# Performance work log

Hardware: AMD Instinct MI355X
Metric: run time of the kernel (lower is better)

The kernel has to match this reference:

```python
import jax, jax.numpy as jnp
import numpy as np

D = 128       # embedding dim; n_phi == D is forced by the module (n_phi = phi.shape[0])
NE = 8192     # enroll trials
NT = 8192     # test trials
EPS = 1e-8


def _make_params():
    """Replicates GPLDA.__init__: derive Q_hat, lambda, U_k from phi/sigma via pinv+SVD."""
    rng = np.random.default_rng(0)
    phi = rng.normal(size=(D, D)) * 0.1
    A = rng.normal(size=(D, D))
    sigma = np.eye(D) + 0.01 * (A @ A.T)          # SPD noise covariance
    sigma_ac = phi @ phi.T
    sigma_tot = sigma_ac + sigma
    inv_tot = np.linalg.pinv(sigma_tot)
    inv_sigma = np.linalg.pinv(sigma_tot - sigma_ac @ inv_tot @ sigma_ac)
    Q = inv_tot - inv_sigma
    P = inv_tot @ sigma_ac @ inv_sigma
    U, S, _ = np.linalg.svd(P)
    n_phi = D
    U_k = U[:, :n_phi]                            # (D, n_phi)
    Q_hat = U_k.T @ Q @ U_k                       # (n_phi, n_phi)
    lam = S[:n_phi]                               # diag of lambda_v
    W = rng.normal(size=(D, D)) / np.sqrt(D)      # whitening matrix
    miu = rng.normal(size=(D,))                   # global mean
    return W, miu, lam, U_k, Q_hat


def setup_inputs() -> dict:
    key = jax.random.key(0)
    k1, k2 = jax.random.split(key)
    W, miu, lam, U_k, Q_hat = _make_params()
    f32 = jnp.float32
    return {
        "x_enroll": jax.random.normal(k1, (NE, D), dtype=f32),
        "x_test": jax.random.normal(k2, (NT, D), dtype=f32),
        "W": jnp.asarray(W, f32),
        "miu": jnp.asarray(miu, f32),
        "lam": jnp.asarray(lam, f32),
        "U_k": jnp.asarray(U_k, f32),
        "Q_hat": jnp.asarray(Q_hat, f32),
    }


def _project(x, miu, W, U_k):
    # x: (N, D) -> projected (n_phi, N)
    xt = x.T - miu[:, None]                       # (D, N) per-feature mean subtraction
    norm = jnp.sqrt(jnp.sum(xt * xt, axis=0))     # per-sample L2 norm (over features)
    xt = xt / (norm + EPS)                        # length-normalize each column
    return U_k.T @ (W.T @ xt)                     # (n_phi, N)


def reference(x_enroll, x_test, W, miu, lam, U_k, Q_hat):
    xe = _project(x_enroll, miu, W, U_k)          # (n_phi, NE)
    xt = _project(x_test, miu, W, U_k)            # (n_phi, NT)
    # diag(xe.T @ Q_hat @ xe) without forming the NxN product
    score_h1 = jnp.sum(xe * (Q_hat @ xe), axis=0)               # (NE,)
    score_h2 = jnp.sum(xt * (Q_hat @ xt), axis=0)               # (NT,)
    # 2 * xe.T @ diag(lam) @ xt
    score_h1h2 = 2.0 * jnp.einsum('kn,k,km->nm', xe, lam, xt)   # (NE, NT)
    return score_h1h2 + score_h1[:, None] + score_h2[None, :]
```

## Files before the change

kernel.cpp:

```cpp
#include <hip/hip_runtime.h>
#include <math.h>

#define D 128
#define NE 8192
#define NT 8192
#define KEXT 384
#define SB 16

typedef __bf16 bf16x8 __attribute__((ext_vector_type(8)));
typedef float f32x4 __attribute__((ext_vector_type(4)));

__device__ __forceinline__ unsigned short f32_to_bf16(float f) {
  unsigned int u = __float_as_uint(f);
  u += 0x7FFFu + ((u >> 16) & 1u);
  return (unsigned short)(u >> 16);
}
__device__ __forceinline__ float bf16_to_f32(unsigned short h) {
  return __uint_as_float(((unsigned int)h) << 16);
}

#define GLOAD_LDS16(g, l)                                                      \
  __builtin_amdgcn_global_load_lds(                                            \
      (__attribute__((address_space(1))) const void*)(g),                      \
      (__attribute__((address_space(3))) void*)(l), 16, 0, 0)

__global__ __launch_bounds__(128) void prep_M(const float* __restrict__ W,
                                              const float* __restrict__ U,
                                              float* __restrict__ M) {
  const int d = blockIdx.x;
  const int k = threadIdx.x;
  const float* Wr = W + d * D;
  float acc = 0.f;
#pragma unroll 8
  for (int c = 0; c < D; ++c) acc += Wr[c] * U[c * D + k];
  M[d * D + k] = acc;
}

__global__ __launch_bounds__(128) void project_kernel(
    const float* __restrict__ Xe, const float* __restrict__ Xt,
    const float* __restrict__ miu, const float* __restrict__ M,
    const float* __restrict__ Qh, const float* __restrict__ lam,
    unsigned short* __restrict__ Aext, unsigned short* __restrict__ Bext,
    float* __restrict__ s1, float* __restrict__ s2) {
  const int t = threadIdx.x;
  const int mode = blockIdx.y;
  const int n0 = blockIdx.x * SB;
  const float* X = mode ? Xt : Xe;
  unsigned short* Ext = mode ? Bext : Aext;
  float* sc = mode ? s2 : s1;

  __shared__ __align__(16) float V[D][20];
  __shared__ __align__(16) float Y[D][20];
  __shared__ float rn[SB];

  const float mu = miu[t];
#pragma unroll
  for (int i = 0; i < SB; ++i)
    V[t][i] = X[(size_t)(n0 + i) * D + t] - mu;
  __syncthreads();

  if (t < SB) {
    float s = 0.f;
#pragma unroll 8
    for (int d = 0; d < D; ++d) { float v = V[d][t]; s += v * v; }
    rn[t] = 1.0f / (sqrtf(s) + 1e-8f);
  }
  __syncthreads();

  float y[SB];
#pragma unroll
  for (int s = 0; s < SB; ++s) y[s] = 0.f;
  {
    const float* Mc = M + t;
#pragma unroll 4
    for (int d = 0; d < D; ++d) {
      float m = Mc[d * D];
#pragma unroll
      for (int s4 = 0; s4 < SB / 4; ++s4) {
        float4 v = *(const float4*)&V[d][s4 * 4];
        y[s4 * 4 + 0] += m * v.x;
        y[s4 * 4 + 1] += m * v.y;
        y[s4 * 4 + 2] += m * v.z;
        y[s4 * 4 + 3] += m * v.w;
      }
    }
  }
#pragma unroll
  for (int s = 0; s < SB; ++s) y[s] *= rn[s];

#pragma unroll
  for (int s4 = 0; s4 < SB / 4; ++s4) {
    float4 v;
    v.x = y[s4 * 4 + 0]; v.y = y[s4 * 4 + 1];
    v.z = y[s4 * 4 + 2]; v.w = y[s4 * 4 + 3];
    *(float4*)&Y[t][s4 * 4] = v;
  }
  __syncthreads();

  float z[SB];
#pragma unroll
  for (int s = 0; s < SB; ++s) z[s] = 0.f;
  {
    const float* Qc = Qh + t;
#pragma unroll 4
    for (int d = 0; d < D; ++d) {
      float q = Qc[d * D];
#pragma unroll
      for (int s4 = 0; s4 < SB / 4; ++s4) {
        float4 v = *(const float4*)&Y[d][s4 * 4];
        z[s4 * 4 + 0] += q * v.x;
        z[s4 * 4 + 1] += q * v.y;
        z[s4 * 4 + 2] += q * v.z;
        z[s4 * 4 + 3] += q * v.w;
      }
    }
  }

#pragma unroll
  for (int s = 0; s < SB; ++s) V[t][s] = y[s] * z[s];
  __syncthreads();
  for (int st = 64; st >= 1; st >>= 1) {
    if (t < st) {
#pragma unroll
      for (int s = 0; s < SB; ++s) V[t][s] += V[t + st][s];
    }
    __syncthreads();
  }
  if (t < SB) sc[n0 + t] = V[0][t];

  const float scale = mode ? 1.0f : 2.0f * lam[t];
#pragma unroll
  for (int s = 0; s < SB; ++s) {
    float w = y[s] * scale;
    unsigned short hi = f32_to_bf16(w);
    unsigned short lo = f32_to_bf16(w - bf16_to_f32(hi));
    size_t base = (size_t)(n0 + s) * KEXT;
    Ext[base + t]         = hi;
    Ext[base + D + t]     = mode ? lo : hi;
    Ext[base + 2 * D + t] = mode ? hi : lo;
  }
}

__global__ __launch_bounds__(256) void gemm_score(
    const unsigned short* __restrict__ A,
    const unsigned short* __restrict__ B,
    const float* __restrict__ s1, const float* __restrict__ s2,
    float* __restrict__ C) {
  __shared__ __align__(16) unsigned short As[128 * 32];
  __shared__ __align__(16) unsigned short Bs[128 * 32];

  const int t = threadIdx.x;
  const int l = t & 63;
  const int w = t >> 6;
  const int wr = w >> 1;
  const int wc = w & 1;
  const int bm0 = blockIdx.y * 128;
  const int bn0 = blockIdx.x * 128;

  f32x4 acc[4][4];
  const f32x4 zero = {0.f, 0.f, 0.f, 0.f};
#pragma unroll
  for (int m = 0; m < 4; ++m)
#pragma unroll
    for (int n = 0; n < 4; ++n) acc[m][n] = zero;

  const int srow = t >> 2;
  const int scol = (t & 3) * 8;
  const int rr = l & 15;
  const int kgo = (l >> 4) * 8;

  for (int kt = 0; kt < KEXT / 32; ++kt) {
#pragma unroll
    for (int j = 0; j < 2; ++j) {
      const unsigned short* ga =
          A + (size_t)(bm0 + j * 64 + srow) * KEXT + kt * 32 + scol;
      GLOAD_LDS16(ga, As + j * 2048 + t * 8);
      const unsigned short* gb =
          B + (size_t)(bn0 + j * 64 + srow) * KEXT + kt * 32 + scol;
      GLOAD_LDS16(gb, Bs + j * 2048 + t * 8);
    }
    __syncthreads();

    bf16x8 af[4], bf[4];
#pragma unroll
    for (int m = 0; m < 4; ++m)
      af[m] = *(const bf16x8*)(As + (wr * 64 + m * 16 + rr) * 32 + kgo);
#pragma unroll
    for (int n = 0; n < 4; ++n)
      bf[n] = *(const bf16x8*)(Bs + (wc * 64 + n * 16 + rr) * 32 + kgo);

#pragma unroll
    for (int m = 0; m < 4; ++m)
#pragma unroll
      for (int n = 0; n < 4; ++n)
        acc[m][n] =
            __builtin_amdgcn_mfma_f32_16x16x32_bf16(af[m], bf[n], acc[m][n], 0, 0, 0);
    __syncthreads();
  }

  const int rq = l >> 4;
  float s2v[4];
#pragma unroll
  for (int n = 0; n < 4; ++n) s2v[n] = s2[bn0 + wc * 64 + n * 16 + rr];
#pragma unroll
  for (int m = 0; m < 4; ++m) {
#pragma unroll
    for (int r = 0; r < 4; ++r) {
      const int row = bm0 + wr * 64 + m * 16 + rq * 4 + r;
      const float s1v = s1[row];
      float* cp = C + (size_t)row * NT + bn0 + wc * 64 + rr;
#pragma unroll
      for (int n = 0; n < 4; ++n) cp[n * 16] = acc[m][n][r] + s1v + s2v[n];
    }
  }
}

extern "C" void kernel_launch(void* const* d_in, const int* in_sizes, int n_in,
                              void* d_out, int out_size, void* d_ws, size_t ws_size,
                              hipStream_t stream) {
  const float* x_enroll = (const float*)d_in[0];
  const float* x_test   = (const float*)d_in[1];
  const float* W        = (const float*)d_in[2];
  const float* miu      = (const float*)d_in[3];
  const float* lam      = (const float*)d_in[4];
  const float* U_k      = (const float*)d_in[5];
  const float* Q_hat    = (const float*)d_in[6];
  float* out = (float*)d_out;

  char* ws = (char*)d_ws;
  float* M  = (float*)ws;
  float* s1 = (float*)(ws + 65536);
  float* s2 = (float*)(ws + 98304);
  unsigned short* Aext = (unsigned short*)(ws + 131072);
  unsigned short* Bext = (unsigned short*)(ws + 131072 + 6291456);

  prep_M<<<dim3(D), dim3(D), 0, stream>>>(W, U_k, M);
  project_kernel<<<dim3(NE / SB, 2), dim3(128), 0, stream>>>(
      x_enroll, x_test, miu, M, Q_hat, lam, Aext, Bext, s1, s2);
  gemm_score<<<dim3(NT / 128, NE / 128), dim3(256), 0, stream>>>(
      Aext, Bext, s1, s2, out);
}
```

Baseline: 358.5 us.

## Pre-swizzle operands into MFMA fragment layout and load directly to registers

```diff
diff --git a/kernel.cpp b/kernel.cpp
--- a/kernel.cpp
+++ b/kernel.cpp
@@ -5,6 +5,7 @@
 #define NE 8192
 #define NT 8192
 #define KEXT 384
+#define NKB (KEXT / 32)
 #define SB 16
 
 typedef __bf16 bf16x8 __attribute__((ext_vector_type(8)));
@@ -18,11 +19,6 @@
 __device__ __forceinline__ float bf16_to_f32(unsigned short h) {
   return __uint_as_float(((unsigned int)h) << 16);
 }
-
-#define GLOAD_LDS16(g, l)                                                      \
-  __builtin_amdgcn_global_load_lds(                                            \
-      (__attribute__((address_space(1))) const void*)(g),                      \
-      (__attribute__((address_space(3))) void*)(l), 16, 0, 0)
 
 __global__ __launch_bounds__(128) void prep_M(const float* __restrict__ W,
                                               const float* __restrict__ U,
@@ -44,7 +40,8 @@
     float* __restrict__ s1, float* __restrict__ s2) {
   const int t = threadIdx.x;
   const int mode = blockIdx.y;
-  const int n0 = blockIdx.x * SB;
+  const int R = blockIdx.x;
+  const int n0 = R * SB;
   const float* X = mode ? Xt : Xe;
   unsigned short* Ext = mode ? Bext : Aext;
   float* sc = mode ? s2 : s1;
@@ -52,6 +49,8 @@
   __shared__ __align__(16) float V[D][20];
   __shared__ __align__(16) float Y[D][20];
   __shared__ float rn[SB];
+  __shared__ __align__(16) unsigned short H[SB][136];
+  __shared__ __align__(16) unsigned short L[SB][136];
 
   const float mu = miu[t];
 #pragma unroll
@@ -134,10 +133,25 @@
     float w = y[s] * scale;
     unsigned short hi = f32_to_bf16(w);
     unsigned short lo = f32_to_bf16(w - bf16_to_f32(hi));
-    size_t base = (size_t)(n0 + s) * KEXT;
-    Ext[base + t]         = hi;
-    Ext[base + D + t]     = mode ? lo : hi;
-    Ext[base + 2 * D + t] = mode ? hi : lo;
+    H[s][t] = hi;
+    L[s][t] = lo;
+  }
+  __syncthreads();
+
+  uint4* outc = (uint4*)Ext + (size_t)R * 768;
+#pragma unroll
+  for (int i = 0; i < 6; ++i) {
+    const int c = i * 128 + t;
+    const int kb = c >> 6;
+    const int sec = kb >> 2;
+    const int koct = (c >> 4) & 3;
+    const int s = c & 15;
+    const int kin = ((kb & 3) << 5) | (koct << 3);
+    const unsigned short* src;
+    if (sec == 0)      src = &H[s][kin];
+    else if (sec == 1) src = mode ? &L[s][kin] : &H[s][kin];
+    else               src = mode ? &H[s][kin] : &L[s][kin];
+    outc[c] = *(const uint4*)src;
   }
 }
 
@@ -146,16 +160,19 @@
     const unsigned short* __restrict__ B,
     const float* __restrict__ s1, const float* __restrict__ s2,
     float* __restrict__ C) {
-  __shared__ __align__(16) unsigned short As[128 * 32];
-  __shared__ __align__(16) unsigned short Bs[128 * 32];
+  const int bid = blockIdx.x;
+  const int xcd = bid & 7;
+  const int q = bid >> 3;
+  const int bx = q >> 3;
+  const int by = (xcd << 3) | (q & 7);
+  const int bm0 = by * 128;
+  const int bn0 = bx * 128;
 
   const int t = threadIdx.x;
   const int l = t & 63;
   const int w = t >> 6;
   const int wr = w >> 1;
   const int wc = w & 1;
-  const int bm0 = blockIdx.y * 128;
-  const int bn0 = blockIdx.x * 128;
 
   f32x4 acc[4][4];
   const f32x4 zero = {0.f, 0.f, 0.f, 0.f};
@@ -164,40 +181,35 @@
 #pragma unroll
     for (int n = 0; n < 4; ++n) acc[m][n] = zero;
 
-  const int srow = t >> 2;
-  const int scol = (t & 3) * 8;
-  const int rr = l & 15;
-  const int kgo = (l >> 4) * 8;
-
-  for (int kt = 0; kt < KEXT / 32; ++kt) {
-#pragma unroll
-    for (int j = 0; j < 2; ++j) {
-      const unsigned short* ga =
-          A + (size_t)(bm0 + j * 64 + srow) * KEXT + kt * 32 + scol;
-      GLOAD_LDS16(ga, As + j * 2048 + t * 8);
-      const unsigned short* gb =
-          B + (size_t)(bn0 + j * 64 + srow) * KEXT + kt * 32 + scol;
-      GLOAD_LDS16(gb, Bs + j * 2048 + t * 8);
-    }
-    __syncthreads();
-
-    bf16x8 af[4], bf[4];
-#pragma unroll
-    for (int m = 0; m < 4; ++m)
-      af[m] = *(const bf16x8*)(As + (wr * 64 + m * 16 + rr) * 32 + kgo);
-#pragma unroll
-    for (int n = 0; n < 4; ++n)
-      bf[n] = *(const bf16x8*)(Bs + (wc * 64 + n * 16 + rr) * 32 + kgo);
-
+  const unsigned short* pa = A + ((size_t)((bm0 >> 4) + wr * 4) * NKB) * 512 + l * 8;
+  const unsigned short* pb = B + ((size_t)((bn0 >> 4) + wc * 4) * NKB) * 512 + l * 8;
+
+  bf16x8 af[2][4], bf[2][4];
+#pragma unroll
+  for (int m = 0; m < 4; ++m) {
+    af[0][m] = *(const bf16x8*)(pa + m * (NKB * 512));
+    bf[0][m] = *(const bf16x8*)(pb + m * (NKB * 512));
+  }
+
+#pragma unroll
+  for (int kt = 0; kt < NKB; ++kt) {
+    const int cur = kt & 1, nxt = cur ^ 1;
+    if (kt < NKB - 1) {
+#pragma unroll
+      for (int m = 0; m < 4; ++m) {
+        af[nxt][m] = *(const bf16x8*)(pa + m * (NKB * 512) + (kt + 1) * 512);
+        bf[nxt][m] = *(const bf16x8*)(pb + m * (NKB * 512) + (kt + 1) * 512);
+      }
+    }
 #pragma unroll
     for (int m = 0; m < 4; ++m)
 #pragma unroll
       for (int n = 0; n < 4; ++n)
         acc[m][n] =
-            __builtin_amdgcn_mfma_f32_16x16x32_bf16(af[m], bf[n], acc[m][n], 0, 0, 0);
-    __syncthreads();
-  }
-
+            __builtin_amdgcn_mfma_f32_16x16x32_bf16(af[cur][m], bf[cur][n], acc[m][n], 0, 0, 0);
+  }
+
+  const int rr = l & 15;
   const int rq = l >> 4;
   float s2v[4];
 #pragma unroll
@@ -237,6 +249,5 @@
   prep_M<<<dim3(D), dim3(D), 0, stream>>>(W, U_k, M);
   project_kernel<<<dim3(NE / SB, 2), dim3(128), 0, stream>>>(
       x_enroll, x_test, miu, M, Q_hat, lam, Aext, Bext, s1, s2);
-  gemm_score<<<dim3(NT / 128, NE / 128), dim3(256), 0, stream>>>(
-      Aext, Bext, s1, s2, out);
-}
+  gemm_score<<<dim3(4096), dim3(256), 0, stream>>>(Aext, Bext, s1, s2, out);
+}
```

New measurement: 371.6 us. +3.6%, slower.
